# Kernel tuning notes

Hardware: AMD Instinct MI355X
Metric: run time of the kernel (lower is better)

## Reference

```python
import jax, jax.numpy as jnp
import numpy as np

X_SIZE = 256
H_SIZE = 512
N_CHILDREN = 32768


def setup_inputs() -> dict:
    key = jax.random.key(0)
    ks = jax.random.split(key, 7)
    x = jax.random.normal(ks[0], (X_SIZE,), dtype=jnp.float32)
    hs = jax.random.normal(ks[1], (N_CHILDREN, H_SIZE), dtype=jnp.float32)
    cs = jax.random.normal(ks[2], (N_CHILDREN, H_SIZE), dtype=jnp.float32)
    # xavier-uniform-ish init for weights, zeros for biases
    def xavier(k, shape):
        fan_in, fan_out = shape[-1], shape[-2]
        limit = float(np.sqrt(6.0 / (fan_in + fan_out)))
        return jax.random.uniform(k, shape, jnp.float32, -limit, limit)
    w_iou = xavier(ks[3], (3, H_SIZE, X_SIZE))
    u_iou = xavier(ks[4], (3, H_SIZE, H_SIZE))
    b_iou = jnp.zeros((3, H_SIZE), jnp.float32)
    w_f = xavier(ks[5], (H_SIZE, X_SIZE))
    u_f = xavier(ks[6], (H_SIZE, H_SIZE))
    b_f = jnp.zeros((H_SIZE, 1), jnp.float32)
    return {"x": x, "hs": hs, "cs": cs, "w_iou": w_iou, "u_iou": u_iou,
            "b_iou": b_iou, "w_f": w_f, "u_f": u_f, "b_f": b_f}


def reference(x, hs, cs, w_iou, u_iou, b_iou, w_f, u_f, b_f):
    # Child-sum Tree-LSTM cell for a single node.
    h_sum = hs.sum(axis=0)                                    # (h,)
    iou = (jnp.einsum('khx,x->kh', w_iou, x)
           + jnp.einsum('khg,g->kh', u_iou, h_sum)
           + b_iou)                                            # (3, h)
    i, o, u = iou[0], iou[1], iou[2]
    # fs: (h, n_children) forget gates, one per child
    fs = (w_f @ x)[:, None] + jnp.einsum('hg,ng->hn', u_f, hs) + b_f
    i = jax.nn.sigmoid(i)
    o = jax.nn.sigmoid(o)
    fs = jax.nn.sigmoid(fs)
    u = jnp.tanh(u)
    c = i * u + jnp.sum(fs * cs.T, axis=1)                    # (h,)
    h = o * jnp.tanh(c)
    return (h, c)
```

## Files before the change

### kernel.cpp

```cpp
#include <hip/hip_runtime.h>
#include <stdint.h>
#include <stddef.h>

#define H 512
#define XD 256
#define NCHLD 32768
#define NB 32
#define MROWS 256
#define NSHARD 32

#define WS_PREF 0
#define WS_IOU  512
#define WS_CACC 2048
#define WS_HSUM 18432
#define WS_UF16 34816

typedef float f32x4 __attribute__((ext_vector_type(4)));
typedef _Float16 f16x8 __attribute__((ext_vector_type(8)));

__device__ __forceinline__ float sigm(float x) { return 1.0f / (1.0f + __expf(-x)); }

__global__ __launch_bounds__(256) void k0_setup(const float* __restrict__ x,
                                                const float* __restrict__ w_f,
                                                const float* __restrict__ b_f,
                                                const float* __restrict__ u_f,
                                                float* __restrict__ ws) {
    const int b = blockIdx.x;
    if (b < 256) {
        const int i = (b * 256 + threadIdx.x) * 4;
        float4 v = *(const float4*)(u_f + i);
        _Float16 h0 = (_Float16)v.x, h1 = (_Float16)v.y;
        _Float16 h2 = (_Float16)v.z, h3 = (_Float16)v.w;
        _Float16* dst = (_Float16*)(ws + WS_UF16) + i;
        dst[0] = h0; dst[1] = h1; dst[2] = h2; dst[3] = h3;
    } else {
        const int gid = (b - 256) * 256 + threadIdx.x;
        const int row = gid >> 2;
        const int part = gid & 3;
        const float4* wr = (const float4*)(w_f + (size_t)row * XD) + part * 16;
        const float4* xv = (const float4*)x + part * 16;
        float acc = 0.0f;
#pragma unroll 4
        for (int i = 0; i < 16; ++i) {
            float4 a = wr[i], c = xv[i];
            acc += a.x * c.x + a.y * c.y + a.z * c.z + a.w * c.w;
        }
        acc += __shfl_xor(acc, 1);
        acc += __shfl_xor(acc, 2);
        if (part == 0) ws[WS_PREF + row] = acc + b_f[row];
        float4 z = make_float4(0.f, 0.f, 0.f, 0.f);
#pragma unroll
        for (int t = 0; t < 4; ++t)
            ((float4*)ws)[512 + gid * 4 + t] = z;
    }
}

__global__ __launch_bounds__(256, 4) void k2_main(const float* __restrict__ hs,
                                                  const float* __restrict__ cs,
                                                  float* __restrict__ ws) {
    __shared__ _Float16 Bs[NB * H];
    __shared__ float hsum_l[H];

    const _Float16* uf16 = (const _Float16*)(ws + WS_UF16);
    const float* pre_f = ws + WS_PREF;
    const int bid   = blockIdx.x;
    const int ntile = bid >> 1;
    const int mtile = bid & 1;
    const int c0    = ntile * NB;
    const int r0    = mtile * MROWS;
    float* c_acc = ws + WS_CACC + (bid & (NSHARD - 1)) * H;

    const int tid  = threadIdx.x;
    const int wid  = tid >> 6;
    const int lane = tid & 63;
    const int fc   = lane & 15;
    const int q    = lane >> 4;

    hsum_l[tid] = 0.0f;
    hsum_l[tid + 256] = 0.0f;
    __syncthreads();

    {
        const float* g0 = hs + (size_t)(c0 + wid * 8) * H + lane * 8;
        _Float16* wbase = Bs + (size_t)(wid * 8) * H + ((lane ^ 0) * 0);
        float4 ha = make_float4(0.f, 0.f, 0.f, 0.f);
        float4 hb = make_float4(0.f, 0.f, 0.f, 0.f);
#pragma unroll
        for (int half = 0; half < 2; ++half) {
            float4 ra[4], rb[4];
#pragma unroll
            for (int j = 0; j < 4; ++j) {
                const int cj = half * 4 + j;
                ra[j] = *(const float4*)(g0 + (size_t)cj * H);
                rb[j] = *(const float4*)(g0 + (size_t)cj * H + 4);
            }
#pragma unroll
            for (int j = 0; j < 4; ++j) {
                const int cj = half * 4 + j;
                f16x8 hv;
                hv[0] = (_Float16)ra[j].x; hv[1] = (_Float16)ra[j].y;
                hv[2] = (_Float16)ra[j].z; hv[3] = (_Float16)ra[j].w;
                hv[4] = (_Float16)rb[j].x; hv[5] = (_Float16)rb[j].y;
                hv[6] = (_Float16)rb[j].z; hv[7] = (_Float16)rb[j].w;
                *(f16x8*)(Bs + (size_t)(wid * 8 + cj) * H + ((lane ^ cj) << 3)) = hv;
                ha.x += ra[j].x; ha.y += ra[j].y; ha.z += ra[j].z; ha.w += ra[j].w;
                hb.x += rb[j].x; hb.y += rb[j].y; hb.z += rb[j].z; hb.w += rb[j].w;
            }
        }
        if (mtile == 0) {
            float* hd = &hsum_l[lane * 8];
            atomicAdd(hd + 0, ha.x); atomicAdd(hd + 1, ha.y);
            atomicAdd(hd + 2, ha.z); atomicAdd(hd + 3, ha.w);
            atomicAdd(hd + 4, hb.x); atomicAdd(hd + 5, hb.y);
            atomicAdd(hd + 6, hb.z); atomicAdd(hd + 7, hb.w);
        }
    }
    __syncthreads();

    if (mtile == 0) {
        float* shard = ws + WS_HSUM + (ntile & (NSHARD - 1)) * H;
        atomicAdd(&shard[tid], hsum_l[tid]);
        atomicAdd(&shard[tid + 256], hsum_l[tid + 256]);
    }

    f32x4 acc[4][2];
    const f32x4 vzero = {0.0f, 0.0f, 0.0f, 0.0f};
#pragma unroll
    for (int rt = 0; rt < 4; ++rt) {
        acc[rt][0] = vzero;
        acc[rt][1] = vzero;
    }

    const _Float16* abase = uf16 + (size_t)(r0 + wid * 64 + fc) * H + q * 8;

#pragma unroll
    for (int kk = 0; kk < 16; ++kk) {
        f16x8 af[4];
#pragma unroll
        for (int rt = 0; rt < 4; ++rt)
            af[rt] = *(const f16x8*)(abase + (size_t)rt * 16 * H + kk * 32);
        f16x8 bf[2];
#pragma unroll
        for (int ct = 0; ct < 2; ++ct)
            bf[ct] = *(const f16x8*)(Bs + (size_t)(ct * 16 + fc) * H + (((kk * 4 + q) ^ (fc & 7)) << 3));
#pragma unroll
        for (int ct = 0; ct < 2; ++ct)
#pragma unroll
            for (int rt = 0; rt < 4; ++rt)
                acc[rt][ct] = __builtin_amdgcn_mfma_f32_16x16x32_f16(af[rt], bf[ct], acc[rt][ct], 0, 0, 0);
    }

#pragma unroll
    for (int rt = 0; rt < 4; ++rt) {
        const int rglob = r0 + wid * 64 + rt * 16 + q * 4;
        float4 pf = *(const float4*)(pre_f + rglob);
        f32x4 csum = vzero;
#pragma unroll
        for (int ct = 0; ct < 2; ++ct) {
            const int child = c0 + ct * 16 + fc;
            float4 cv = *(const float4*)(cs + (size_t)child * H + rglob);
            csum[0] += sigm(acc[rt][ct][0] + pf.x) * cv.x;
            csum[1] += sigm(acc[rt][ct][1] + pf.y) * cv.y;
            csum[2] += sigm(acc[rt][ct][2] + pf.z) * cv.z;
            csum[3] += sigm(acc[rt][ct][3] + pf.w) * cv.w;
        }
#pragma unroll
        for (int m = 1; m <= 8; m <<= 1) {
            csum[0] += __shfl_xor(csum[0], m); csum[1] += __shfl_xor(csum[1], m);
            csum[2] += __shfl_xor(csum[2], m); csum[3] += __shfl_xor(csum[3], m);
        }
        if (fc == 0) {
            atomicAdd(&c_acc[rglob + 0], csum[0]); atomicAdd(&c_acc[rglob + 1], csum[1]);
            atomicAdd(&c_acc[rglob + 2], csum[2]); atomicAdd(&c_acc[rglob + 3], csum[3]);
        }
    }
}

__global__ __launch_bounds__(256) void k3_iou(const float* __restrict__ x,
                                              const float* __restrict__ w_iou,
                                              const float* __restrict__ u_iou,
                                              const float* __restrict__ b_iou,
                                              float* __restrict__ ws) {
    __shared__ float h_red[H];
    const int tid = threadIdx.x;
    {
        float a0 = 0.0f, a1 = 0.0f;
#pragma unroll 8
        for (int s = 0; s < NSHARD; ++s) {
            a0 += ws[WS_HSUM + s * H + tid * 2 + 0];
            a1 += ws[WS_HSUM + s * H + tid * 2 + 1];
        }
        h_red[tid * 2 + 0] = a0;
        h_red[tid * 2 + 1] = a1;
    }
    __syncthreads();

    const int gid = blockIdx.x * 256 + tid;
    const int row = gid >> 4;
    const int part = gid & 15;
    float acc = 0.0f;
    const float4* wr = (const float4*)(w_iou + (size_t)row * XD) + part * 4;
    const float4* xv = (const float4*)x + part * 4;
#pragma unroll
    for (int i = 0; i < 4; ++i) {
        float4 a = wr[i], b = xv[i];
        acc += a.x * b.x + a.y * b.y + a.z * b.z + a.w * b.w;
    }
    const float4* ur = (const float4*)(u_iou + (size_t)row * H) + part * 8;
    const float4* hv = (const float4*)h_red + part * 8;
#pragma unroll
    for (int i = 0; i < 8; ++i) {
        float4 a = ur[i], b = hv[i];
        acc += a.x * b.x + a.y * b.y + a.z * b.z + a.w * b.w;
    }
    acc += __shfl_xor(acc, 1);
    acc += __shfl_xor(acc, 2);
    acc += __shfl_xor(acc, 4);
    acc += __shfl_xor(acc, 8);
    if (part == 0) ws[WS_IOU + row] = acc + b_iou[row];
}

__global__ __launch_bounds__(512) void k4_fin(const float* __restrict__ ws,
                                              float* __restrict__ out) {
    const int h = threadIdx.x;
    float cacc = 0.0f;
#pragma unroll 8
    for (int s = 0; s < NSHARD; ++s) cacc += ws[WS_CACC + s * H + h];
    const float i = sigm(ws[WS_IOU + h]);
    const float o = sigm(ws[WS_IOU + 512 + h]);
    const float u = tanhf(ws[WS_IOU + 1024 + h]);
    const float c = i * u + cacc;
    out[h]       = o * tanhf(c);
    out[512 + h] = c;
}

extern "C" void kernel_launch(void* const* d_in, const int* in_sizes, int n_in,
                              void* d_out, int out_size, void* d_ws, size_t ws_size,
                              hipStream_t stream) {
    const float* x     = (const float*)d_in[0];
    const float* hs    = (const float*)d_in[1];
    const float* cs    = (const float*)d_in[2];
    const float* w_iou = (const float*)d_in[3];
    const float* u_iou = (const float*)d_in[4];
    const float* b_iou = (const float*)d_in[5];
    const float* w_f   = (const float*)d_in[6];
    const float* u_f   = (const float*)d_in[7];
    const float* b_f   = (const float*)d_in[8];
    float* ws  = (float*)d_ws;
    float* out = (float*)d_out;

    k0_setup<<<264, 256, 0, stream>>>(x, w_f, b_f, u_f, ws);
    k2_main<<<(NCHLD / NB) * 2, 256, 0, stream>>>(hs, cs, ws);
    k3_iou<<<96, 256, 0, stream>>>(x, w_iou, u_iou, b_iou, ws);
    k4_fin<<<1, 512, 0, stream>>>(ws, out);
}
```

Baseline: 243.5 us.

## Load hs directly to LDS as fp32 and merge M-tiles into 512-thread blocks

The main kernel now uses 512-thread blocks that each cover all 512 rows for a 32-child tile, instead of two 256-thread blocks that each read the same hs tile. The hs tile is copied straight into LDS with global_load_lds using an XOR-swizzled layout, and is kept in fp32 and converted to fp16 at fragment-load time. The h-sum is computed from LDS without shared atomics, and A fragments are register double-buffered. This halves hs global reads and removes register staging, at the cost of twice the LDS footprint (64KB per block), which limits occupancy.

```diff
diff --git a/kernel.cpp b/kernel.cpp
--- a/kernel.cpp
+++ b/kernel.cpp
@@ -6,7 +6,6 @@
 #define XD 256
 #define NCHLD 32768
 #define NB 32
-#define MROWS 256
 #define NSHARD 32
 
 #define WS_PREF 0
@@ -19,6 +18,12 @@
 typedef _Float16 f16x8 __attribute__((ext_vector_type(8)));
 
 __device__ __forceinline__ float sigm(float x) { return 1.0f / (1.0f + __expf(-x)); }
+
+__device__ __forceinline__ void gload_lds16(const float* g, void* l) {
+    __builtin_amdgcn_global_load_lds((const __attribute__((address_space(1))) void*)g,
+                                     (__attribute__((address_space(3))) void*)l,
+                                     16, 0, 0);
+}
 
 __global__ __launch_bounds__(256) void k0_setup(const float* __restrict__ x,
                                                 const float* __restrict__ w_f,
@@ -29,10 +34,9 @@
     if (b < 256) {
         const int i = (b * 256 + threadIdx.x) * 4;
         float4 v = *(const float4*)(u_f + i);
-        _Float16 h0 = (_Float16)v.x, h1 = (_Float16)v.y;
-        _Float16 h2 = (_Float16)v.z, h3 = (_Float16)v.w;
         _Float16* dst = (_Float16*)(ws + WS_UF16) + i;
-        dst[0] = h0; dst[1] = h1; dst[2] = h2; dst[3] = h3;
+        dst[0] = (_Float16)v.x; dst[1] = (_Float16)v.y;
+        dst[2] = (_Float16)v.z; dst[3] = (_Float16)v.w;
     } else {
         const int gid = (b - 256) * 256 + threadIdx.x;
         const int row = gid >> 2;
@@ -55,20 +59,17 @@
     }
 }
 
-__global__ __launch_bounds__(256, 4) void k2_main(const float* __restrict__ hs,
+__global__ __launch_bounds__(512, 4) void k2_main(const float* __restrict__ hs,
                                                   const float* __restrict__ cs,
                                                   float* __restrict__ ws) {
-    __shared__ _Float16 Bs[NB * H];
-    __shared__ float hsum_l[H];
+    __shared__ float Bs[NB * H];
 
     const _Float16* uf16 = (const _Float16*)(ws + WS_UF16);
     const float* pre_f = ws + WS_PREF;
-    const int bid   = blockIdx.x;
-    const int ntile = bid >> 1;
-    const int mtile = bid & 1;
-    const int c0    = ntile * NB;
-    const int r0    = mtile * MROWS;
-    float* c_acc = ws + WS_CACC + (bid & (NSHARD - 1)) * H;
+    const int bid = blockIdx.x;
+    const int c0  = bid * NB;
+    float* c_acc   = ws + WS_CACC + (bid & (NSHARD - 1)) * H;
+    float* h_shard = ws + WS_HSUM + (bid & (NSHARD - 1)) * H;
 
     const int tid  = threadIdx.x;
     const int wid  = tid >> 6;
@@ -76,83 +77,74 @@
     const int fc   = lane & 15;
     const int q    = lane >> 4;
 
-    hsum_l[tid] = 0.0f;
-    hsum_l[tid + 256] = 0.0f;
+#pragma unroll
+    for (int t = 0; t < 8; ++t) {
+        const int idx  = wid * 8 + t;
+        const int r    = idx >> 1;
+        const int half = idx & 1;
+        const int slot_g = half * 64 + (lane ^ (r & 7));
+        gload_lds16(hs + (size_t)(c0 + r) * H + slot_g * 4,
+                    (char*)Bs + (size_t)idx * 1024);
+    }
     __syncthreads();
 
     {
-        const float* g0 = hs + (size_t)(c0 + wid * 8) * H + lane * 8;
-        _Float16* wbase = Bs + (size_t)(wid * 8) * H + ((lane ^ 0) * 0);
-        float4 ha = make_float4(0.f, 0.f, 0.f, 0.f);
-        float4 hb = make_float4(0.f, 0.f, 0.f, 0.f);
-#pragma unroll
-        for (int half = 0; half < 2; ++half) {
-            float4 ra[4], rb[4];
-#pragma unroll
-            for (int j = 0; j < 4; ++j) {
-                const int cj = half * 4 + j;
-                ra[j] = *(const float4*)(g0 + (size_t)cj * H);
-                rb[j] = *(const float4*)(g0 + (size_t)cj * H + 4);
-            }
-#pragma unroll
-            for (int j = 0; j < 4; ++j) {
-                const int cj = half * 4 + j;
-                f16x8 hv;
-                hv[0] = (_Float16)ra[j].x; hv[1] = (_Float16)ra[j].y;
-                hv[2] = (_Float16)ra[j].z; hv[3] = (_Float16)ra[j].w;
-                hv[4] = (_Float16)rb[j].x; hv[5] = (_Float16)rb[j].y;
-                hv[6] = (_Float16)rb[j].z; hv[7] = (_Float16)rb[j].w;
-                *(f16x8*)(Bs + (size_t)(wid * 8 + cj) * H + ((lane ^ cj) << 3)) = hv;
-                ha.x += ra[j].x; ha.y += ra[j].y; ha.z += ra[j].z; ha.w += ra[j].w;
-                hb.x += rb[j].x; hb.y += rb[j].y; hb.z += rb[j].z; hb.w += rb[j].w;
-            }
-        }
-        if (mtile == 0) {
-            float* hd = &hsum_l[lane * 8];
-            atomicAdd(hd + 0, ha.x); atomicAdd(hd + 1, ha.y);
-            atomicAdd(hd + 2, ha.z); atomicAdd(hd + 3, ha.w);
-            atomicAdd(hd + 4, hb.x); atomicAdd(hd + 5, hb.y);
-            atomicAdd(hd + 6, hb.z); atomicAdd(hd + 7, hb.w);
-        }
-    }
-    __syncthreads();
-
-    if (mtile == 0) {
-        float* shard = ws + WS_HSUM + (ntile & (NSHARD - 1)) * H;
-        atomicAdd(&shard[tid], hsum_l[tid]);
-        atomicAdd(&shard[tid + 256], hsum_l[tid + 256]);
+        const int sl = tid >> 2, wd = tid & 3;
+        float hsum = 0.0f;
+#pragma unroll
+        for (int ch = 0; ch < NB; ++ch)
+            hsum += *(const float*)((const char*)Bs + ch * 2048 + ((sl ^ (ch & 7)) << 4) + wd * 4);
+        atomicAdd(&h_shard[tid], hsum);
     }
 
     f32x4 acc[4][2];
     const f32x4 vzero = {0.0f, 0.0f, 0.0f, 0.0f};
 #pragma unroll
-    for (int rt = 0; rt < 4; ++rt) {
-        acc[rt][0] = vzero;
-        acc[rt][1] = vzero;
-    }
-
-    const _Float16* abase = uf16 + (size_t)(r0 + wid * 64 + fc) * H + q * 8;
+    for (int rt = 0; rt < 4; ++rt) { acc[rt][0] = vzero; acc[rt][1] = vzero; }
+
+    const _Float16* abase = uf16 + (size_t)(wid * 64 + fc) * H + q * 8;
+
+    f16x8 af[4], afn[4];
+#pragma unroll
+    for (int rt = 0; rt < 4; ++rt)
+        af[rt] = *(const f16x8*)(abase + (size_t)rt * 16 * H);
 
 #pragma unroll
     for (int kk = 0; kk < 16; ++kk) {
-        f16x8 af[4];
-#pragma unroll
-        for (int rt = 0; rt < 4; ++rt)
-            af[rt] = *(const f16x8*)(abase + (size_t)rt * 16 * H + kk * 32);
+        if (kk < 15) {
+#pragma unroll
+            for (int rt = 0; rt < 4; ++rt)
+                afn[rt] = *(const f16x8*)(abase + (size_t)rt * 16 * H + (kk + 1) * 32);
+        }
+        const int s0 = kk * 8 + q * 2;
         f16x8 bf[2];
 #pragma unroll
-        for (int ct = 0; ct < 2; ++ct)
-            bf[ct] = *(const f16x8*)(Bs + (size_t)(ct * 16 + fc) * H + (((kk * 4 + q) ^ (fc & 7)) << 3));
+        for (int ct = 0; ct < 2; ++ct) {
+            const int child = ct * 16 + fc;
+            const int sl0 = s0 ^ (fc & 7);
+            f32x4 v0 = *(const f32x4*)((const char*)Bs + child * 2048 + (sl0 << 4));
+            f32x4 v1 = *(const f32x4*)((const char*)Bs + child * 2048 + ((sl0 ^ 1) << 4));
+            f16x8 bv;
+            bv[0] = (_Float16)v0[0]; bv[1] = (_Float16)v0[1];
+            bv[2] = (_Float16)v0[2]; bv[3] = (_Float16)v0[3];
+            bv[4] = (_Float16)v1[0]; bv[5] = (_Float16)v1[1];
+            bv[6] = (_Float16)v1[2]; bv[7] = (_Float16)v1[3];
+            bf[ct] = bv;
+        }
 #pragma unroll
         for (int ct = 0; ct < 2; ++ct)
 #pragma unroll
             for (int rt = 0; rt < 4; ++rt)
                 acc[rt][ct] = __builtin_amdgcn_mfma_f32_16x16x32_f16(af[rt], bf[ct], acc[rt][ct], 0, 0, 0);
+        if (kk < 15) {
+#pragma unroll
+            for (int rt = 0; rt < 4; ++rt) af[rt] = afn[rt];
+        }
     }
 
 #pragma unroll
     for (int rt = 0; rt < 4; ++rt) {
-        const int rglob = r0 + wid * 64 + rt * 16 + q * 4;
+        const int rglob = wid * 64 + rt * 16 + q * 4;
         float4 pf = *(const float4*)(pre_f + rglob);
         f32x4 csum = vzero;
 #pragma unroll
@@ -250,7 +242,7 @@
     float* out = (float*)d_out;
 
     k0_setup<<<264, 256, 0, stream>>>(x, w_f, b_f, u_f, ws);
-    k2_main<<<(NCHLD / NB) * 2, 256, 0, stream>>>(hs, cs, ws);
+    k2_main<<<NCHLD / NB, 512, 0, stream>>>(hs, cs, ws);
     k3_iou<<<96, 256, 0, stream>>>(x, w_iou, u_iou, b_iou, ws);
     k4_fin<<<1, 512, 0, stream>>>(ws, out);
 }
```

New measurement: 229.9 us. 1.06x faster.
